# Performance work log

Hardware: AMD Instinct MI355X
Metric: run time of the kernel (lower is better)

## Reference

```python
import jax, jax.numpy as jnp
import numpy as np

CONF_THRES = 0.7
IOU_THRES = 0.45
MAX_DET = 512  # padded per-image candidate count after confidence top-k


def setup_inputs() -> dict:
    key = jax.random.key(0)
    # raw YOLO-style predictions: [B, N, 9] = cx,cy,w,h,obj,cls,pitch,yaw,roll
    pred = jax.random.uniform(key, (64, 100800, 9), dtype=jnp.float32)
    return {"pred": pred}


def _xywh2xyxy(b):
    cx, cy, w, h = b[..., 0], b[..., 1], b[..., 2], b[..., 3]
    return jnp.stack([cx - w * 0.5, cy - h * 0.5, cx + w * 0.5, cy + h * 0.5], axis=-1)


def _pairwise_iou(boxes):
    # boxes: [B, K, 4] in xyxy -> [B, K, K] IoU matrix
    lt = jnp.maximum(boxes[:, :, None, :2], boxes[:, None, :, :2])
    rb = jnp.minimum(boxes[:, :, None, 2:], boxes[:, None, :, 2:])
    wh = jnp.clip(rb - lt, 0.0)
    inter = wh[..., 0] * wh[..., 1]
    area = (boxes[..., 2] - boxes[..., 0]) * (boxes[..., 3] - boxes[..., 1])
    union = area[:, :, None] + area[:, None, :] - inter
    return inter / (union + 1e-7)


def reference(pred):
    """Batched YOLOv5-style NMS (single class) with DirectMHP euler angles.

    Returns [B, MAX_DET, 9]: x1,y1,x2,y2,conf,class,pitch,yaw,roll;
    suppressed / below-threshold slots are zeroed (fixed-shape padding).
    """
    K = MAX_DET
    conf = pred[..., 4] * pred[..., 5]                  # obj * cls prob
    score = jnp.where(conf > CONF_THRES, conf, 0.0)     # threshold filter
    top_scores, idx = jax.lax.top_k(score, K)           # sorted desc, [B, K]

    take = lambda a: jnp.take_along_axis(a, idx[..., None], axis=1)
    boxes = _xywh2xyxy(take(pred[..., :4]))             # [B, K, 4]
    angles = take(pred[..., 6:9])                       # [B, K, 3]

    iou = _pairwise_iou(boxes)                          # [B, K, K]
    keep0 = top_scores > CONF_THRES                     # [B, K]
    rng = jnp.arange(K)

    def body(i, keep):
        # greedy suppression: box i (if still kept) kills later boxes with IoU > thr
        keep_i = jnp.take(keep, i, axis=1)[:, None]     # [B, 1]
        iou_i = jnp.take(iou, i, axis=1)                # [B, K]
        sup = (iou_i > IOU_THRES) & keep_i & (rng > i)[None, :]
        return keep & ~sup

    keep = jax.lax.fori_loop(0, K, body, keep0)

    cls = jnp.zeros_like(top_scores)
    out = jnp.concatenate(
        [boxes, top_scores[..., None], cls[..., None], angles], axis=-1
    )  # [B, K, 9]
    return out * keep[..., None].astype(out.dtype)
```

## Files before the change

### kernel.cpp

```cpp
#include <hip/hip_runtime.h>
#include <hip/hip_bf16.h>

#define N_ANCH 100800
#define BATCH 64
#define KTOP 512
#define CNT_STRIDE 64

__global__ void zero_cnt_kernel(int* __restrict__ cnt) {
    if (threadIdx.x < BATCH) cnt[threadIdx.x * CNT_STRIDE] = 0;
}

__global__ void filter_kernel(const float* __restrict__ pred,
                              unsigned long long* __restrict__ cand,
                              int* __restrict__ cnt, int cap) {
    __shared__ float tile[256 * 9];
    __shared__ int s_wbase[4];
    __shared__ int s_blkcnt;
    __shared__ int s_gbase;

    const int b  = blockIdx.y;
    const int r0 = blockIdx.x * 256;
    const int rows = min(256, N_ANCH - r0);
    const size_t base = ((size_t)b * N_ANCH + r0) * 9;

    if (threadIdx.x == 0) s_blkcnt = 0;

    const int nf4 = (rows * 9) >> 2;
    const float4* __restrict__ src = (const float4*)(pred + base);
    float4* dst4 = (float4*)tile;
    for (int f = threadIdx.x; f < nf4; f += 256) dst4[f] = src[f];
    __syncthreads();

    const int t = threadIdx.x;
    const int wid = t >> 6, lane = t & 63;
    bool has = false;
    unsigned long long key = 0;
    if (t < rows) {
        float s = tile[t * 9 + 4] * tile[t * 9 + 5];
        if (s > 0.7f) {
            has = true;
            unsigned int sb = __float_as_uint(s);
            unsigned int gi = (unsigned int)(r0 + t);
            key = ((unsigned long long)sb << 32) | (unsigned long long)(~gi);
        }
    }

    unsigned long long m = __ballot(has);
    if (lane == 0) s_wbase[wid] = atomicAdd(&s_blkcnt, __popcll(m));
    __syncthreads();
    if (t == 0) s_gbase = atomicAdd(&cnt[b * CNT_STRIDE], s_blkcnt);
    __syncthreads();

    if (has) {
        int rank = __popcll(m & ((1ull << lane) - 1ull));
        int pos = s_gbase + s_wbase[wid] + rank;
        if (pos < cap) cand[(size_t)b * cap + pos] = key;
    }
}

__global__ void __launch_bounds__(1024)
nms_kernel(const float* __restrict__ pred,
           const unsigned long long* __restrict__ cand,
           const int* __restrict__ cnt,
           float* __restrict__ out, int cap) {
#pragma clang fp contract(off)
    __shared__ int hist[2048];
    __shared__ int csf[256];
    __shared__ unsigned long long sel[1024];
    __shared__ float4 boxes[KTOP];
    __shared__ float sc[KTOP];
    __shared__ int ids[KTOP];
    __shared__ unsigned long long msk[KTOP][8];
    __shared__ unsigned long long rmw[8];
    __shared__ int s_bstar, s_nsel;

    const int b = blockIdx.x;
    const int t = threadIdx.x;
    const int c = min(cnt[b * CNT_STRIDE], cap);
    const unsigned long long* __restrict__ cb = cand + (size_t)b * cap;

    for (int i = t; i < 2048; i += 1024) hist[i] = 0;
    sel[t] = 0;
    if (t == 0) { s_nsel = 0; s_bstar = 0; }
    __syncthreads();

    for (int i = t; i < c; i += 1024) {
        unsigned int sb = (unsigned int)(cb[i] >> 32);
        atomicAdd(&hist[(sb >> 12) & 0x7FF], 1);
    }
    __syncthreads();

    {
        if (t < 256) {
            int s = 0;
            #pragma unroll
            for (int j = 0; j < 8; ++j) s += hist[t * 8 + j];
            csf[t] = s;
        }
        __syncthreads();
        for (int off = 1; off < 256; off <<= 1) {
            int v2 = 0;
            if (t < 256) v2 = csf[t] + ((t + off < 256) ? csf[t + off] : 0);
            __syncthreads();
            if (t < 256) csf[t] = v2;
            __syncthreads();
        }
        if (t < 256) {
            int cs_t  = csf[t];
            int cs_t1 = (t == 255) ? 0 : csf[t + 1];
            if (cs_t >= KTOP && cs_t1 < KTOP) {
                int cum = cs_t1, bstar = t * 8;
                for (int j = 7; j >= 0; --j) {
                    cum += hist[t * 8 + j];
                    if (cum >= KTOP) { bstar = t * 8 + j; break; }
                }
                s_bstar = bstar;
            }
        }
        __syncthreads();
    }

    const int bstar = s_bstar;
    for (int i = t; i < c; i += 1024) {
        unsigned long long k = cb[i];
        unsigned int sb = (unsigned int)(k >> 32);
        if ((int)((sb >> 12) & 0x7FF) >= bstar) {
            int p = atomicAdd(&s_nsel, 1);
            if (p < 1024) sel[p] = k;
        }
    }
    __syncthreads();
    const int v = min(s_nsel, KTOP);

    for (int k = 2; k <= 1024; k <<= 1) {
        for (int j = k >> 1; j > 0; j >>= 1) {
            __syncthreads();
            if (t < 512) {
                int i0 = ((t & ~(j - 1)) << 1) | (t & (j - 1));
                int i1 = i0 | j;
                unsigned long long a = sel[i0], bb = sel[i1];
                bool up = ((i0 & k) == 0);
                if ((a < bb) == up) { sel[i0] = bb; sel[i1] = a; }
            }
        }
    }
    __syncthreads();

    if (t < KTOP) {
        int s = t;
        float4 bx = make_float4(0.f, 0.f, 0.f, 0.f);
        float scv = 0.f;
        int gid = -1;
        if (s < v) {
            unsigned long long k = sel[s];
            scv = __uint_as_float((unsigned int)(k >> 32));
            gid = (int)(~(unsigned int)(k & 0xFFFFFFFFull));
            const float* row = pred + ((size_t)b * N_ANCH + gid) * 9;
            float cx = row[0], cy = row[1], w = row[2], h = row[3];
            float hw = w * 0.5f, hh = h * 0.5f;
            bx = make_float4(cx - hw, cy - hh, cx + hw, cy + hh);
        }
        boxes[s] = bx;
        sc[s] = scv;
        ids[s] = gid;
    }
    __syncthreads();

    {
        const int i = t & 511;
        const int wb = (t >> 9) << 2;
        float4 bi = boxes[i];
        float ai = (bi.z - bi.x) * (bi.w - bi.y);
        #pragma unroll
        for (int kk = 0; kk < 4; ++kk) {
            int w = wb + kk;
            int j0 = w << 6;
            unsigned long long mword = 0;
            if (j0 + 63 > i) {
                #pragma unroll 8
                for (int jj = 0; jj < 64; ++jj) {
                    float4 bj = boxes[j0 + jj];
                    float xx1 = fmaxf(bi.x, bj.x);
                    float yy1 = fmaxf(bi.y, bj.y);
                    float xx2 = fminf(bi.z, bj.z);
                    float yy2 = fminf(bi.w, bj.w);
                    float ww = fmaxf(xx2 - xx1, 0.f);
                    float hh = fmaxf(yy2 - yy1, 0.f);
                    float inter = ww * hh;
                    float aj = (bj.z - bj.x) * (bj.w - bj.y);
                    float uni = ai + aj - inter;
                    float iou = inter / (uni + 1e-7f);
                    mword |= (unsigned long long)(iou > 0.45f) << jj;
                }
                if (j0 <= i) mword &= (~0ull) << (i - j0 + 1);
            }
            msk[i][w] = mword;
        }
    }
    __syncthreads();

    if (t == 0) {
        unsigned long long rm[8] = {0, 0, 0, 0, 0, 0, 0, 0};
        for (int w = 0; w < 8 && (w << 6) < v; ++w) {
            int rem = v - (w << 6);
            unsigned long long valid = (rem >= 64) ? ~0ull : ((1ull << rem) - 1ull);
            unsigned long long alive = ~rm[w] & valid;
            while (alive) {
                int bit = __ffsll(alive) - 1;
                int i = (w << 6) + bit;
                #pragma unroll
                for (int u = 0; u < 8; ++u) rm[u] |= msk[i][u];
                alive &= ~rm[w];
                alive &= (bit == 63) ? 0ull : (~0ull << (bit + 1));
            }
        }
        #pragma unroll
        for (int u = 0; u < 8; ++u) rmw[u] = rm[u];
    }
    __syncthreads();

    if (t < KTOP) {
        int s = t;
        float* o = out + ((size_t)b * KTOP + s) * 9;
        bool keep = (sc[s] > 0.7f) && !((rmw[s >> 6] >> (s & 63)) & 1ull);
        if (keep) {
            float4 bx = boxes[s];
            const float* row = pred + ((size_t)b * N_ANCH + ids[s]) * 9;
            o[0] = bx.x; o[1] = bx.y; o[2] = bx.z; o[3] = bx.w;
            o[4] = sc[s]; o[5] = 0.f;
            o[6] = row[6]; o[7] = row[7]; o[8] = row[8];
        } else {
            o[0] = 0.f; o[1] = 0.f; o[2] = 0.f; o[3] = 0.f;
            o[4] = 0.f; o[5] = 0.f; o[6] = 0.f; o[7] = 0.f; o[8] = 0.f;
        }
    }
}

extern "C" void kernel_launch(void* const* d_in, const int* in_sizes, int n_in,
                              void* d_out, int out_size, void* d_ws, size_t ws_size,
                              hipStream_t stream) {
    const float* pred = (const float*)d_in[0];
    float* out = (float*)d_out;

    int* cnt = (int*)d_ws;
    unsigned long long* cand = (unsigned long long*)((char*)d_ws + BATCH * CNT_STRIDE * 4);

    int cap = 8192;
    size_t head = (size_t)BATCH * CNT_STRIDE * 4;
    size_t need = head + (size_t)BATCH * cap * sizeof(unsigned long long);
    if (ws_size < need) {
        cap = (int)((ws_size > head ? (ws_size - head) : 0) /
                    (BATCH * sizeof(unsigned long long)));
    }

    zero_cnt_kernel<<<1, 64, 0, stream>>>(cnt);

    dim3 g1((N_ANCH + 255) / 256, BATCH);
    filter_kernel<<<g1, 256, 0, stream>>>(pred, cand, cnt, cap);

    nms_kernel<<<BATCH, 1024, 0, stream>>>(pred, cand, cnt, out, cap);
}
```

Before: 405.2 us.

## Read scores directly in filter, use wave-shuffle histogram scan and bitonic sort

The filter kernel drops the full-row LDS tiling and has each thread read only the obj and cls floats of its own row, using 1024-thread blocks. The NMS kernel keeps candidate keys in registers and replaces the LDS prefix scan used for the threshold bin with wave shuffles. Bitonic stages with stride below 64 now use __shfl_xor instead of LDS plus barriers. Each thread in the IoU pass handles two rows so each boxes[j] load is reused, and the sc/ids arrays are dropped in favour of decoding sel. The strided two-float loads may waste bandwidth compared with the coalesced float4 copy, and kreg[8] assumes at most 8192 candidates per image.

```diff
diff --git a/kernel.cpp b/kernel.cpp
--- a/kernel.cpp
+++ b/kernel.cpp
@@ -10,37 +10,32 @@
     if (threadIdx.x < BATCH) cnt[threadIdx.x * CNT_STRIDE] = 0;
 }
 
-__global__ void filter_kernel(const float* __restrict__ pred,
-                              unsigned long long* __restrict__ cand,
-                              int* __restrict__ cnt, int cap) {
-    __shared__ float tile[256 * 9];
-    __shared__ int s_wbase[4];
+__global__ void __launch_bounds__(1024)
+filter_kernel(const float* __restrict__ pred,
+              unsigned long long* __restrict__ cand,
+              int* __restrict__ cnt, int cap) {
+#pragma clang fp contract(off)
+    __shared__ int s_wbase[16];
     __shared__ int s_blkcnt;
     __shared__ int s_gbase;
 
-    const int b  = blockIdx.y;
-    const int r0 = blockIdx.x * 256;
-    const int rows = min(256, N_ANCH - r0);
-    const size_t base = ((size_t)b * N_ANCH + r0) * 9;
-
-    if (threadIdx.x == 0) s_blkcnt = 0;
-
-    const int nf4 = (rows * 9) >> 2;
-    const float4* __restrict__ src = (const float4*)(pred + base);
-    float4* dst4 = (float4*)tile;
-    for (int f = threadIdx.x; f < nf4; f += 256) dst4[f] = src[f];
-    __syncthreads();
-
+    const int b = blockIdx.y;
     const int t = threadIdx.x;
+    const int r = blockIdx.x * 1024 + t;
     const int wid = t >> 6, lane = t & 63;
+
+    if (t == 0) s_blkcnt = 0;
+    __syncthreads();
+
     bool has = false;
     unsigned long long key = 0;
-    if (t < rows) {
-        float s = tile[t * 9 + 4] * tile[t * 9 + 5];
+    if (r < N_ANCH) {
+        const float* row = pred + ((size_t)b * N_ANCH + r) * 9;
+        float s = row[4] * row[5];
         if (s > 0.7f) {
             has = true;
             unsigned int sb = __float_as_uint(s);
-            unsigned int gi = (unsigned int)(r0 + t);
+            unsigned int gi = (unsigned int)r;
             key = ((unsigned long long)sb << 32) | (unsigned long long)(~gi);
         }
     }
@@ -65,11 +60,8 @@
            float* __restrict__ out, int cap) {
 #pragma clang fp contract(off)
     __shared__ int hist[2048];
-    __shared__ int csf[256];
     __shared__ unsigned long long sel[1024];
     __shared__ float4 boxes[KTOP];
-    __shared__ float sc[KTOP];
-    __shared__ int ids[KTOP];
     __shared__ unsigned long long msk[KTOP][8];
     __shared__ unsigned long long rmw[8];
     __shared__ int s_bstar, s_nsel;
@@ -84,117 +76,154 @@
     if (t == 0) { s_nsel = 0; s_bstar = 0; }
     __syncthreads();
 
-    for (int i = t; i < c; i += 1024) {
-        unsigned int sb = (unsigned int)(cb[i] >> 32);
-        atomicAdd(&hist[(sb >> 12) & 0x7FF], 1);
-    }
-    __syncthreads();
-
-    {
-        if (t < 256) {
-            int s = 0;
-            #pragma unroll
-            for (int j = 0; j < 8; ++j) s += hist[t * 8 + j];
-            csf[t] = s;
-        }
-        __syncthreads();
-        for (int off = 1; off < 256; off <<= 1) {
-            int v2 = 0;
-            if (t < 256) v2 = csf[t] + ((t + off < 256) ? csf[t + off] : 0);
-            __syncthreads();
-            if (t < 256) csf[t] = v2;
-            __syncthreads();
-        }
-        if (t < 256) {
-            int cs_t  = csf[t];
-            int cs_t1 = (t == 255) ? 0 : csf[t + 1];
-            if (cs_t >= KTOP && cs_t1 < KTOP) {
-                int cum = cs_t1, bstar = t * 8;
-                for (int j = 7; j >= 0; --j) {
-                    cum += hist[t * 8 + j];
-                    if (cum >= KTOP) { bstar = t * 8 + j; break; }
-                }
-                s_bstar = bstar;
-            }
-        }
-        __syncthreads();
-    }
-
-    const int bstar = s_bstar;
+    unsigned long long kreg[8];
+    int nk = 0;
     for (int i = t; i < c; i += 1024) {
         unsigned long long k = cb[i];
-        unsigned int sb = (unsigned int)(k >> 32);
-        if ((int)((sb >> 12) & 0x7FF) >= bstar) {
-            int p = atomicAdd(&s_nsel, 1);
-            if (p < 1024) sel[p] = k;
+        kreg[nk++] = k;
+        atomicAdd(&hist[(int)((k >> 44) & 0x7FF)], 1);
+    }
+    __syncthreads();
+
+    if (t < 64) {
+        const int4* h4 = (const int4*)hist;
+        int S = 0;
+        #pragma unroll
+        for (int mch = 0; mch < 8; ++mch) {
+            int4 v = h4[(t << 3) + mch];
+            S += v.x + v.y + v.z + v.w;
+        }
+        #pragma unroll
+        for (int off = 1; off < 64; off <<= 1) {
+            int v2 = __shfl_down(S, off);
+            if (t + off < 64) S += v2;
+        }
+        unsigned long long m1 = __ballot(S >= KTOP);
+        int bstar = 0;
+        if (m1) {
+            int lstar = 63 - __clzll(m1);
+            int nxt = __shfl(S, (lstar + 1) & 63);
+            int carry = (lstar < 63) ? nxt : 0;
+            int C = (t < 32) ? hist[(lstar << 5) + t] : 0;
+            #pragma unroll
+            for (int off = 1; off < 32; off <<= 1) {
+                int v2 = __shfl_down(C, off);
+                if (t + off < 32) C += v2;
+            }
+            C += carry;
+            unsigned long long m2 = __ballot((t < 32) && (C >= KTOP));
+            int jstar = 63 - __clzll(m2);
+            bstar = (lstar << 5) + jstar;
+        }
+        if (t == 0) s_bstar = bstar;
+    }
+    __syncthreads();
+
+    const int bstar = s_bstar;
+    #pragma unroll
+    for (int u = 0; u < 8; ++u) {
+        if (u < nk) {
+            unsigned long long k = kreg[u];
+            if ((int)((k >> 44) & 0x7FF) >= bstar) {
+                int p = atomicAdd(&s_nsel, 1);
+                if (p < 1024) sel[p] = k;
+            }
         }
     }
     __syncthreads();
     const int v = min(s_nsel, KTOP);
 
-    for (int k = 2; k <= 1024; k <<= 1) {
-        for (int j = k >> 1; j > 0; j >>= 1) {
-            __syncthreads();
-            if (t < 512) {
-                int i0 = ((t & ~(j - 1)) << 1) | (t & (j - 1));
-                int i1 = i0 | j;
-                unsigned long long a = sel[i0], bb = sel[i1];
-                bool up = ((i0 & k) == 0);
-                if ((a < bb) == up) { sel[i0] = bb; sel[i1] = a; }
-            }
-        }
-    }
-    __syncthreads();
+    {
+        unsigned long long key = sel[t];
+        for (int k = 2; k <= 1024; k <<= 1) {
+            for (int j = k >> 1; j > 0; j >>= 1) {
+                unsigned long long other;
+                if (j >= 64) {
+                    sel[t] = key;
+                    __syncthreads();
+                    other = sel[t ^ j];
+                    __syncthreads();
+                } else {
+                    other = __shfl_xor(key, j, 64);
+                }
+                bool descSeg = ((t & k) == 0);
+                bool lower   = ((t & j) == 0);
+                bool keepMax = (descSeg == lower);
+                bool takeOther = keepMax ? (other > key) : (other < key);
+                if (takeOther) key = other;
+            }
+        }
+        sel[t] = key;
+        __syncthreads();
+    }
 
     if (t < KTOP) {
-        int s = t;
         float4 bx = make_float4(0.f, 0.f, 0.f, 0.f);
-        float scv = 0.f;
-        int gid = -1;
-        if (s < v) {
-            unsigned long long k = sel[s];
-            scv = __uint_as_float((unsigned int)(k >> 32));
-            gid = (int)(~(unsigned int)(k & 0xFFFFFFFFull));
+        if (t < v) {
+            unsigned long long k = sel[t];
+            int gid = (int)(~(unsigned int)(k & 0xFFFFFFFFull));
             const float* row = pred + ((size_t)b * N_ANCH + gid) * 9;
             float cx = row[0], cy = row[1], w = row[2], h = row[3];
             float hw = w * 0.5f, hh = h * 0.5f;
             bx = make_float4(cx - hw, cy - hh, cx + hw, cy + hh);
         }
-        boxes[s] = bx;
-        sc[s] = scv;
-        ids[s] = gid;
+        boxes[t] = bx;
     }
     __syncthreads();
 
     {
-        const int i = t & 511;
-        const int wb = (t >> 9) << 2;
-        float4 bi = boxes[i];
-        float ai = (bi.z - bi.x) * (bi.w - bi.y);
-        #pragma unroll
-        for (int kk = 0; kk < 4; ++kk) {
-            int w = wb + kk;
-            int j0 = w << 6;
-            unsigned long long mword = 0;
-            if (j0 + 63 > i) {
+        const int q  = t & 255;
+        const int i0 = q << 1, i1 = i0 + 1;
+        const int wp = t >> 8;
+        float4 b0 = boxes[i0], b1 = boxes[i1];
+        float a0 = (b0.z - b0.x) * (b0.w - b0.y);
+        float a1 = (b1.z - b1.x) * (b1.w - b1.y);
+        #pragma unroll
+        for (int s = 0; s < 2; ++s) {
+            const int w = (wp << 1) + s;
+            const int j0 = w << 6;
+            unsigned long long m0 = 0, m1 = 0;
+            if (j0 + 63 > i0) {
                 #pragma unroll 8
                 for (int jj = 0; jj < 64; ++jj) {
                     float4 bj = boxes[j0 + jj];
-                    float xx1 = fmaxf(bi.x, bj.x);
-                    float yy1 = fmaxf(bi.y, bj.y);
-                    float xx2 = fminf(bi.z, bj.z);
-                    float yy2 = fminf(bi.w, bj.w);
-                    float ww = fmaxf(xx2 - xx1, 0.f);
-                    float hh = fmaxf(yy2 - yy1, 0.f);
-                    float inter = ww * hh;
                     float aj = (bj.z - bj.x) * (bj.w - bj.y);
-                    float uni = ai + aj - inter;
-                    float iou = inter / (uni + 1e-7f);
-                    mword |= (unsigned long long)(iou > 0.45f) << jj;
-                }
-                if (j0 <= i) mword &= (~0ull) << (i - j0 + 1);
-            }
-            msk[i][w] = mword;
+                    {
+                        float xx1 = fmaxf(b0.x, bj.x);
+                        float yy1 = fmaxf(b0.y, bj.y);
+                        float xx2 = fminf(b0.z, bj.z);
+                        float yy2 = fminf(b0.w, bj.w);
+                        float ww = fmaxf(xx2 - xx1, 0.f);
+                        float hh = fmaxf(yy2 - yy1, 0.f);
+                        float inter = ww * hh;
+                        float uni = a0 + aj - inter;
+                        float iou = inter / (uni + 1e-7f);
+                        m0 |= (unsigned long long)(iou > 0.45f) << jj;
+                    }
+                    {
+                        float xx1 = fmaxf(b1.x, bj.x);
+                        float yy1 = fmaxf(b1.y, bj.y);
+                        float xx2 = fminf(b1.z, bj.z);
+                        float yy2 = fminf(b1.w, bj.w);
+                        float ww = fmaxf(xx2 - xx1, 0.f);
+                        float hh = fmaxf(yy2 - yy1, 0.f);
+                        float inter = ww * hh;
+                        float uni = a1 + aj - inter;
+                        float iou = inter / (uni + 1e-7f);
+                        m1 |= (unsigned long long)(iou > 0.45f) << jj;
+                    }
+                }
+                if (j0 <= i0) {
+                    int sh = i0 - j0 + 1;
+                    m0 = (sh >= 64) ? 0ull : (m0 & ((~0ull) << sh));
+                }
+                if (j0 <= i1) {
+                    int sh = i1 - j0 + 1;
+                    m1 = (sh >= 64) ? 0ull : (m1 & ((~0ull) << sh));
+                }
+            }
+            msk[i0][w] = m0;
+            msk[i1][w] = m1;
         }
     }
     __syncthreads();
@@ -220,14 +249,16 @@
     __syncthreads();
 
     if (t < KTOP) {
-        int s = t;
-        float* o = out + ((size_t)b * KTOP + s) * 9;
-        bool keep = (sc[s] > 0.7f) && !((rmw[s >> 6] >> (s & 63)) & 1ull);
+        unsigned long long k = sel[t];
+        float scv = __uint_as_float((unsigned int)(k >> 32));
+        float* o = out + ((size_t)b * KTOP + t) * 9;
+        bool keep = (scv > 0.7f) && !((rmw[t >> 6] >> (t & 63)) & 1ull);
         if (keep) {
-            float4 bx = boxes[s];
-            const float* row = pred + ((size_t)b * N_ANCH + ids[s]) * 9;
+            int gid = (int)(~(unsigned int)(k & 0xFFFFFFFFull));
+            float4 bx = boxes[t];
+            const float* row = pred + ((size_t)b * N_ANCH + gid) * 9;
             o[0] = bx.x; o[1] = bx.y; o[2] = bx.z; o[3] = bx.w;
-            o[4] = sc[s]; o[5] = 0.f;
+            o[4] = scv; o[5] = 0.f;
             o[6] = row[6]; o[7] = row[7]; o[8] = row[8];
         } else {
             o[0] = 0.f; o[1] = 0.f; o[2] = 0.f; o[3] = 0.f;
@@ -255,8 +286,8 @@
 
     zero_cnt_kernel<<<1, 64, 0, stream>>>(cnt);
 
-    dim3 g1((N_ANCH + 255) / 256, BATCH);
-    filter_kernel<<<g1, 256, 0, stream>>>(pred, cand, cnt, cap);
+    dim3 g1((N_ANCH + 1023) / 1024, BATCH);
+    filter_kernel<<<g1, 1024, 0, stream>>>(pred, cand, cnt, cap);
 
     nms_kernel<<<BATCH, 1024, 0, stream>>>(pred, cand, cnt, out, cap);
 }
```

Measured after the change: 407.0 us. No clear change (+0.4%).
